# Kernel tuning notes

Hardware: AMD Instinct MI355X
Metric: run time of the kernel (lower is better)

The kernel has to match this reference:

```python
import jax, jax.numpy as jnp
import numpy as np

T = 512  # time_step

def setup_inputs() -> dict:
    key = jax.random.key(0)
    k1, k2, k3 = jax.random.split(key, 3)
    inputs = jax.random.normal(k1, (64, 1024, T), dtype=jnp.float32)
    # Dense stand-in for the ModuleList of Linear(i+1, 1): row i uses cols 0..i.
    # PyTorch Linear init scale ~ U(-1/sqrt(fan_in), 1/sqrt(fan_in)); simple normal is fine for a correctness baseline.
    W = jax.random.normal(k2, (T, T), dtype=jnp.float32) * 0.05
    b = jax.random.normal(k3, (T,), dtype=jnp.float32) * 0.05
    return {"inputs": inputs, "W": W, "b": b}

def reference(inputs, W, b):
    # out[..., i] = sum_{j<=i} inputs[..., j] * W[i, j] + b[i]
    Wtri = jnp.tril(W)  # lower-triangular mask == prefix Linear structure
    return jnp.einsum('bnj,ij->bni', inputs, Wtri) + b
```

## Files before the change

kernel.cpp:

```cpp
#include <hip/hip_runtime.h>
#include <hip/hip_bf16.h>


#define TK 512
#define BM 128
#define BN 128
#define BK 64

typedef __attribute__((ext_vector_type(4))) float f32x4;
typedef __attribute__((ext_vector_type(4))) __bf16 bf16x4;
typedef __attribute__((ext_vector_type(8))) __bf16 bf16x8;

__device__ __forceinline__ void gload_lds16(const void* g, void* l) {
    __builtin_amdgcn_global_load_lds(
        (const __attribute__((address_space(1))) unsigned int*)g,
        (__attribute__((address_space(3))) unsigned int*)l, 16, 0, 0);
}

__global__ __launch_bounds__(256)
void prep_w_kernel(const float* __restrict__ W, __bf16* __restrict__ Wb) {
    const int tid = blockIdx.x * 256 + threadIdx.x;
    const int i  = tid >> 7;
    const int j0 = (tid & 127) * 4;
    f32x4 v = *reinterpret_cast<const f32x4*>(W + (size_t)i * TK + j0);
    bf16x4 o;
    #pragma unroll
    for (int e = 0; e < 4; ++e)
        o[e] = (j0 + e <= i) ? (__bf16)v[e] : (__bf16)0.f;
    *reinterpret_cast<bf16x4*>(Wb + (size_t)i * TK + j0) = o;
}

__global__ __launch_bounds__(256, 3)
void triu_gemm_kernel(const float* __restrict__ X, const __bf16* __restrict__ Wb,
                      const float* __restrict__ bias, float* __restrict__ out) {
    __shared__ float  As[BM][BK];
    __shared__ __bf16 Bs[BN][BK];

    const int bm = blockIdx.x * BM;
    const int n0 = blockIdx.y * BN;
    const int kmax = n0 + BN;

    const int t    = threadIdx.x;
    const int wave = t >> 6;
    const int lane = t & 63;
    const int wr   = wave >> 1;
    const int wc   = wave & 1;
    const int l15  = lane & 15;
    const int l4   = lane >> 4;

    const float* srcA[8]; float* dstA[8];
    #pragma unroll
    for (int i = 0; i < 8; ++i) {
        const int p = i * 256 + t, row = p >> 4, c = p & 15;
        srcA[i] = X + (size_t)(bm + row) * TK + ((c ^ (row & 7)) << 2);
        dstA[i] = &As[0][0] + p * 4;
    }
    const __bf16* srcB[4]; __bf16* dstB[4];
    #pragma unroll
    for (int i = 0; i < 4; ++i) {
        const int p = i * 256 + t, row = p >> 3, c = p & 7;
        srcB[i] = Wb + (size_t)(n0 + row) * TK + ((c ^ (row & 7)) << 3);
        dstB[i] = &Bs[0][0] + p * 8;
    }

    f32x4 acc[4][4];
    #pragma unroll
    for (int m = 0; m < 4; ++m)
        #pragma unroll
        for (int n = 0; n < 4; ++n)
            acc[m][n] = (f32x4){0.f, 0.f, 0.f, 0.f};

    for (int k0 = 0; k0 < kmax; k0 += BK) {
        #pragma unroll
        for (int i = 0; i < 8; ++i) gload_lds16(srcA[i] + k0, dstA[i]);
        #pragma unroll
        for (int i = 0; i < 4; ++i) gload_lds16(srcB[i] + k0, dstB[i]);
        __syncthreads();

        #pragma unroll
        for (int ks = 0; ks < 2; ++ks) {
            bf16x8 a[4], b[4];
            #pragma unroll
            for (int m = 0; m < 4; ++m) {
                const int row = wr * 64 + m * 16 + l15;
                const int c0 = (ks * 8 + l4 * 2)     ^ (row & 7);
                const int c1 = (ks * 8 + l4 * 2 + 1) ^ (row & 7);
                f32x4 v0 = *reinterpret_cast<const f32x4*>(&As[row][c0 * 4]);
                f32x4 v1 = *reinterpret_cast<const f32x4*>(&As[row][c1 * 4]);
                #pragma unroll
                for (int e = 0; e < 4; ++e) a[m][e]     = (__bf16)v0[e];
                #pragma unroll
                for (int e = 0; e < 4; ++e) a[m][4 + e] = (__bf16)v1[e];
            }
            #pragma unroll
            for (int n = 0; n < 4; ++n) {
                const int row = wc * 64 + n * 16 + l15;
                const int c = (ks * 4 + l4) ^ (row & 7);
                b[n] = *reinterpret_cast<const bf16x8*>(&Bs[row][c * 8]);
            }
            #pragma unroll
            for (int m = 0; m < 4; ++m)
                #pragma unroll
                for (int n = 0; n < 4; ++n)
                    acc[m][n] = __builtin_amdgcn_mfma_f32_16x16x32_bf16(
                        a[m], b[n], acc[m][n], 0, 0, 0);
        }
        __syncthreads();
    }

    #pragma unroll
    for (int n = 0; n < 4; ++n) {
        const int col = n0 + wc * 64 + n * 16 + l15;
        const float bv = bias[col];
        #pragma unroll
        for (int m = 0; m < 4; ++m) {
            const int row0 = bm + wr * 64 + m * 16 + l4 * 4;
            #pragma unroll
            for (int j = 0; j < 4; ++j)
                out[(size_t)(row0 + j) * TK + col] = acc[m][n][j] + bv;
        }
    }
}

extern "C" void kernel_launch(void* const* d_in, const int* in_sizes, int n_in,
                              void* d_out, int out_size, void* d_ws, size_t ws_size,
                              hipStream_t stream) {
    const float* X = (const float*)d_in[0];
    const float* W = (const float*)d_in[1];
    const float* b = (const float*)d_in[2];
    float* out = (float*)d_out;
    __bf16* Wb = (__bf16*)d_ws;

    prep_w_kernel<<<256, 256, 0, stream>>>(W, Wb);

    const int M = in_sizes[0] / TK;
    dim3 grid(M / BM, TK / BN);
    triu_gemm_kernel<<<grid, 256, 0, stream>>>(X, Wb, b, out);
}
```

Baseline: 259.3 us.

## Double-buffer LDS tiles with async global-to-LDS prefetch and smaller K step

Shrinks the K tile to 32 and double-buffers the A and B LDS tiles. While computing on one buffer, the next stage's global_load_lds is already in flight, tracked with explicit vmcnt waits and raw barriers. The B tile layout is repacked so two rows share a 64-element swizzled line. The grid is flattened so the four column blocks of the same row tile are adjacent, which should improve L2 reuse of X. The cost is more barriers per unit of K and careful vmcnt accounting that must stay correct.

Measured after the change: 278.3 us. +7.3%, slower.

```diff
diff --git a/kernel.cpp b/kernel.cpp
--- a/kernel.cpp
+++ b/kernel.cpp
@@ -5,7 +5,7 @@
 #define TK 512
 #define BM 128
 #define BN 128
-#define BK 64
+#define BK 32
 
 typedef __attribute__((ext_vector_type(4))) float f32x4;
 typedef __attribute__((ext_vector_type(4))) __bf16 bf16x4;
@@ -33,34 +33,36 @@
 __global__ __launch_bounds__(256, 3)
 void triu_gemm_kernel(const float* __restrict__ X, const __bf16* __restrict__ Wb,
                       const float* __restrict__ bias, float* __restrict__ out) {
-    __shared__ float  As[BM][BK];
-    __shared__ __bf16 Bs[BN][BK];
+    __shared__ float  As[2][BM * BK];
+    __shared__ __bf16 Bs[2][BN * BK];
 
-    const int bm = blockIdx.x * BM;
-    const int n0 = blockIdx.y * BN;
-    const int kmax = n0 + BN;
+    const int bid = blockIdx.x;
+    const int bm = (bid >> 2) * BM;
+    const int n0 = (bid & 3) * BN;
+    const int nt = (n0 + BN) / BK;
 
     const int t    = threadIdx.x;
+    const int lane = t & 63;
     const int wave = t >> 6;
-    const int lane = t & 63;
-    const int wr   = wave >> 1;
-    const int wc   = wave & 1;
-    const int l15  = lane & 15;
-    const int l4   = lane >> 4;
+    const int wr   = wave >> 1, wc = wave & 1;
+    const int l15  = lane & 15, l4 = lane >> 4;
 
-    const float* srcA[8]; float* dstA[8];
-    #pragma unroll
-    for (int i = 0; i < 8; ++i) {
-        const int p = i * 256 + t, row = p >> 4, c = p & 15;
-        srcA[i] = X + (size_t)(bm + row) * TK + ((c ^ (row & 7)) << 2);
-        dstA[i] = &As[0][0] + p * 4;
-    }
-    const __bf16* srcB[4]; __bf16* dstB[4];
+    const float* sA[4]; float* dA[4];
     #pragma unroll
     for (int i = 0; i < 4; ++i) {
-        const int p = i * 256 + t, row = p >> 3, c = p & 7;
-        srcB[i] = Wb + (size_t)(n0 + row) * TK + ((c ^ (row & 7)) << 3);
-        dstB[i] = &Bs[0][0] + p * 8;
+        const int p = i * 256 + t, row = p >> 3, cs = p & 7;
+        const int cl = cs ^ (row & 7);
+        sA[i] = X + (size_t)(bm + row) * TK + cl * 4;
+        dA[i] = &As[0][p * 4];
+    }
+    const __bf16* sB[2]; __bf16* dB[2];
+    #pragma unroll
+    for (int i = 0; i < 2; ++i) {
+        const int p = i * 256 + t, sr = p >> 3, cs = p & 7;
+        const int cl = cs ^ (sr & 7);
+        const int row = sr * 2 + (cl >> 2), kc = cl & 3;
+        sB[i] = Wb + (size_t)(n0 + row) * TK + kc * 8;
+        dB[i] = &Bs[0][p * 8];
     }
 
     f32x4 acc[4][4];
@@ -70,42 +72,56 @@
         for (int n = 0; n < 4; ++n)
             acc[m][n] = (f32x4){0.f, 0.f, 0.f, 0.f};
 
-    for (int k0 = 0; k0 < kmax; k0 += BK) {
+    auto stage = [&](int buf, int tt) {
+        const int k0 = tt * BK;
         #pragma unroll
-        for (int i = 0; i < 8; ++i) gload_lds16(srcA[i] + k0, dstA[i]);
+        for (int i = 0; i < 4; ++i)
+            gload_lds16(sA[i] + k0, dA[i] + buf * (BM * BK));
         #pragma unroll
-        for (int i = 0; i < 4; ++i) gload_lds16(srcB[i] + k0, dstB[i]);
-        __syncthreads();
+        for (int i = 0; i < 2; ++i)
+            gload_lds16(sB[i] + k0, dB[i] + buf * (BN * BK));
+    };
 
+    stage(0, 0);
+    stage(1, 1);
+
+    for (int tt = 0; tt < nt; ++tt) {
+        if (tt + 1 < nt) asm volatile("s_waitcnt vmcnt(6)" ::: "memory");
+        else             asm volatile("s_waitcnt vmcnt(0)" ::: "memory");
+        __builtin_amdgcn_s_barrier();
+        __builtin_amdgcn_sched_barrier(0);
+
+        const int buf = tt & 1;
+        bf16x8 a[4], b[4];
         #pragma unroll
-        for (int ks = 0; ks < 2; ++ks) {
-            bf16x8 a[4], b[4];
+        for (int m = 0; m < 4; ++m) {
+            const int row = wr * 64 + m * 16 + l15;
+            const int c0 = (l4 * 2)     ^ (row & 7);
+            const int c1 = (l4 * 2 + 1) ^ (row & 7);
+            f32x4 v0 = *reinterpret_cast<const f32x4*>(&As[buf][row * BK + c0 * 4]);
+            f32x4 v1 = *reinterpret_cast<const f32x4*>(&As[buf][row * BK + c1 * 4]);
             #pragma unroll
-            for (int m = 0; m < 4; ++m) {
-                const int row = wr * 64 + m * 16 + l15;
-                const int c0 = (ks * 8 + l4 * 2)     ^ (row & 7);
-                const int c1 = (ks * 8 + l4 * 2 + 1) ^ (row & 7);
-                f32x4 v0 = *reinterpret_cast<const f32x4*>(&As[row][c0 * 4]);
-                f32x4 v1 = *reinterpret_cast<const f32x4*>(&As[row][c1 * 4]);
-                #pragma unroll
-                for (int e = 0; e < 4; ++e) a[m][e]     = (__bf16)v0[e];
-                #pragma unroll
-                for (int e = 0; e < 4; ++e) a[m][4 + e] = (__bf16)v1[e];
-            }
+            for (int e = 0; e < 4; ++e) a[m][e]     = (__bf16)v0[e];
             #pragma unroll
-            for (int n = 0; n < 4; ++n) {
-                const int row = wc * 64 + n * 16 + l15;
-                const int c = (ks * 4 + l4) ^ (row & 7);
-                b[n] = *reinterpret_cast<const bf16x8*>(&Bs[row][c * 8]);
-            }
+            for (int e = 0; e < 4; ++e) a[m][4 + e] = (__bf16)v1[e];
+        }
+        #pragma unroll
+        for (int n = 0; n < 4; ++n) {
+            const int row = wc * 64 + n * 16 + l15;
+            const int sr  = row >> 1;
+            const int c   = ((row & 1) * 4 + l4) ^ (sr & 7);
+            b[n] = *reinterpret_cast<const bf16x8*>(&Bs[buf][sr * 64 + c * 8]);
+        }
+        #pragma unroll
+        for (int m = 0; m < 4; ++m)
             #pragma unroll
-            for (int m = 0; m < 4; ++m)
-                #pragma unroll
-                for (int n = 0; n < 4; ++n)
-                    acc[m][n] = __builtin_amdgcn_mfma_f32_16x16x32_bf16(
-                        a[m], b[n], acc[m][n], 0, 0, 0);
-        }
-        __syncthreads();
+            for (int n = 0; n < 4; ++n)
+                acc[m][n] = __builtin_amdgcn_mfma_f32_16x16x32_bf16(
+                    a[m], b[n], acc[m][n], 0, 0, 0);
+
+        __builtin_amdgcn_s_barrier();
+        __builtin_amdgcn_sched_barrier(0);
+        if (tt + 2 < nt) stage(buf, tt + 2);
     }
 
     #pragma unroll
@@ -134,6 +150,5 @@
     prep_w_kernel<<<256, 256, 0, stream>>>(W, Wb);
 
     const int M = in_sizes[0] / TK;
-    dim3 grid(M / BM, TK / BN);
-    triu_gemm_kernel<<<grid, 256, 0, stream>>>(X, Wb, b, out);
+    triu_gemm_kernel<<<(M / BM) * (TK / BN), 256, 0, stream>>>(X, Wb, b, out);
 }
```
